# Optimization experiments

Hardware: AMD Instinct MI355X
Metric: run time of the kernel (lower is better)

Reference implementation:

```python
import jax, jax.numpy as jnp
import numpy as np

NUM_HEADS = 16
EPS = 1e-12  # matches torch F.normalize eps


def _l2norm(t):
    n = jnp.sqrt(jnp.sum(t * t, axis=-1, keepdims=True))
    return t / jnp.maximum(n, EPS)


def setup_inputs() -> dict:
    key = jax.random.key(0)
    kx, kq, kk, kv = jax.random.split(key, 4)
    B, S, E = 2, 2048, 1024
    head_dim = E // NUM_HEADS
    bound = 1.0 / np.sqrt(E)  # nn.Linear default init range
    x = jax.random.normal(kx, (B, S, E), dtype=jnp.float32)
    Wq = jax.random.uniform(kq, (E, E), dtype=jnp.float32, minval=-bound, maxval=bound)
    Wk = jax.random.uniform(kk, (E, E), dtype=jnp.float32, minval=-bound, maxval=bound)
    Wv = jax.random.uniform(kv, (E, E), dtype=jnp.float32, minval=-bound, maxval=bound)
    g_scale = jnp.asarray(np.sqrt(head_dim), dtype=jnp.float32)  # 1/d_k = sqrt(head_dim)
    return {"x": x, "Wq": Wq, "Wk": Wk, "Wv": Wv, "g_scale": g_scale}


def reference(x, Wq, Wk, Wv, g_scale):
    B, S, E = x.shape
    H = NUM_HEADS
    D = E // H
    # projections (torch Linear: x @ W.T), split heads -> [B, H, S, D]
    q = (x @ Wq.T).reshape(B, S, H, D).transpose(0, 2, 1, 3)
    k = (x @ Wk.T).reshape(B, S, H, D).transpose(0, 2, 1, 3)
    v = (x @ Wv.T).reshape(B, S, H, D).transpose(0, 2, 1, 3)
    # qk_norm branch: L2-normalize q, k then learnable scale
    q = _l2norm(q)
    k = _l2norm(k)
    scores = g_scale * jnp.einsum('bhqd,bhkd->bhqk', q, k)  # [B, H, S, S]
    attn = jax.nn.softmax(scores, axis=-1)
    # dropout p=0.0 (eval) -> identity
    out = jnp.einsum('bhqk,bhkd->bhqd', attn, v)  # [B, H, S, D]
    out = out.transpose(0, 2, 1, 3).reshape(B, S, E)
    return out
```

## Files before the change

### kernel.cpp

```cpp
#include <hip/hip_runtime.h>
#include <math.h>

#define NH 16
#define HD 64
#define SEQ 2048
#define BAT 2
#define EMB 1024
#define MTOT (BAT*SEQ)
#define NTOT (3*EMB)

typedef __attribute__((ext_vector_type(8))) short bf16x8;
typedef __attribute__((ext_vector_type(4))) float f32x4;

#define MFMA16(a,b,c) __builtin_amdgcn_mfma_f32_16x16x32_bf16(a,b,c,0,0,0)

__device__ inline short f2bf(float f) {
    union { float f; unsigned u; } x; x.f = f;
    unsigned r = (x.u + 0x7FFF + ((x.u >> 16) & 1)) >> 16;
    return (short)r;
}

__device__ inline float fast_exp2(float x) {
#if __has_builtin(__builtin_amdgcn_exp2f)
    return __builtin_amdgcn_exp2f(x);
#else
    float r; asm("v_exp_f32 %0, %1" : "=v"(r) : "v"(x)); return r;
#endif
}

__device__ inline unsigned pack2bf(float a, float b) {
    union { float f; unsigned u; } x, y; x.f = a; y.f = b;
    return __builtin_amdgcn_perm(y.u + 0x8000u, x.u + 0x8000u, 0x07060302u);
}

typedef const __attribute__((address_space(1))) void* gp_t;
typedef __attribute__((address_space(3))) void* lp_t;
__device__ inline void gload16(const void* g, void* l) {
    __builtin_amdgcn_global_load_lds((gp_t)(uintptr_t)g, (lp_t)(uintptr_t)l, 16, 0, 0);
}

__global__ __launch_bounds__(256) void prep_kernel(
    const float* __restrict__ x, const float* __restrict__ wq,
    const float* __restrict__ wk, const float* __restrict__ wv,
    short* __restrict__ xb, short* __restrict__ wb)
{
    const size_t NX = (size_t)MTOT * EMB;
    const size_t NW = (size_t)EMB * EMB;
    const size_t i4 = ((size_t)blockIdx.x * 256 + threadIdx.x) * 4;
    float4 v; short* dst;
    if (i4 < NX) { v = *(const float4*)(x + i4); dst = xb + i4; }
    else {
        size_t j = i4 - NX;
        const float* s = (j < NW) ? wq : (j < 2 * NW) ? wk : wv;
        v = *(const float4*)(s + (j & (NW - 1)));
        dst = wb + j;
    }
    short4 o; o.x = f2bf(v.x); o.y = f2bf(v.y); o.z = f2bf(v.z); o.w = f2bf(v.w);
    *(short4*)dst = o;
}

__global__ __launch_bounds__(256) void qkv_gemm_fast(
    const short* __restrict__ xb, const short* __restrict__ wb,
    short* __restrict__ qws, short* __restrict__ kws, short* __restrict__ vperm,
    const float* __restrict__ gptr)
{
    __shared__ short As[128 * 64];
    __shared__ short Bs[128 * 64];
    const int m0 = blockIdx.x * 128, n0 = blockIdx.y * 128;
    const int t = threadIdx.x, wave = t >> 6, lane = t & 63;
    const int quad = lane >> 4, l16 = lane & 15;
    const int wm = (wave & 1) * 64, wn = (wave >> 1) * 64;

    const int srow = wave * 32 + (lane >> 3);
    const int scol = ((lane & 7) ^ (srow & 7)) * 8;
    const short* ga = xb + (size_t)(m0 + srow) * EMB + scol;
    const short* gb = wb + (size_t)(n0 + srow) * EMB + scol;
    short* lA = As + (size_t)wave * 2048;
    short* lB = Bs + (size_t)wave * 2048;

    const short* Aa[2]; const short* Ba[2];
#pragma unroll
    for (int ks = 0; ks < 2; ++ks) {
        const int pc = (ks * 32 + quad * 8) ^ ((l16 & 7) * 8);
        Aa[ks] = As + (wm + l16) * 64 + pc;
        Ba[ks] = Bs + (wn + l16) * 64 + pc;
    }

    f32x4 acc[4][4] = {};

    for (int k0 = 0; k0 < EMB; k0 += 64) {
#pragma unroll
        for (int j = 0; j < 4; ++j) {
            gload16(ga + k0 + (size_t)j * 8 * EMB, lA + j * 512);
            gload16(gb + k0 + (size_t)j * 8 * EMB, lB + j * 512);
        }
        __syncthreads();
#pragma unroll
        for (int ks = 0; ks < 2; ++ks) {
            bf16x8 af[4], bfr[4];
#pragma unroll
            for (int i = 0; i < 4; ++i) af[i]  = *(const bf16x8*)(Aa[ks] + i * 1024);
#pragma unroll
            for (int i = 0; i < 4; ++i) bfr[i] = *(const bf16x8*)(Ba[ks] + i * 1024);
#pragma unroll
            for (int mf = 0; mf < 4; ++mf)
#pragma unroll
                for (int nf = 0; nf < 4; ++nf)
                    acc[mf][nf] = MFMA16(af[mf], bfr[nf], acc[mf][nf]);
        }
        __syncthreads();
    }

    const int mat = n0 >> 10;
    if (mat < 2) {
        const float scale = (mat == 0) ? gptr[0] * 1.4426950408889634f : 1.0f;
        float inv[4][4];
#pragma unroll
        for (int mf = 0; mf < 4; ++mf)
#pragma unroll
            for (int reg = 0; reg < 4; ++reg) {
                float ss = 0.f;
#pragma unroll
                for (int nf = 0; nf < 4; ++nf) { float v = acc[mf][nf][reg]; ss += v * v; }
                ss += __shfl_xor(ss, 1, 16);
                ss += __shfl_xor(ss, 2, 16);
                ss += __shfl_xor(ss, 4, 16);
                ss += __shfl_xor(ss, 8, 16);
                inv[mf][reg] = scale / fmaxf(sqrtf(ss), 1e-12f);
            }
        short* outp = (mat == 0) ? qws : kws;
#pragma unroll
        for (int mf = 0; mf < 4; ++mf)
#pragma unroll
            for (int nf = 0; nf < 4; ++nf) {
                const int cw = (n0 & 1023) + wn + nf * 16 + l16;
                const int h = cw >> 6, d = cw & 63;
#pragma unroll
                for (int reg = 0; reg < 4; ++reg) {
                    const int s = m0 + wm + mf * 16 + quad * 4 + reg;
                    const int b = s >> 11, sl = s & (SEQ - 1);
                    outp[(((size_t)(b * NH + h) * SEQ + sl) * HD) + d] =
                        f2bf(acc[mf][nf][reg] * inv[mf][reg]);
                }
            }
    } else {
#pragma unroll
        for (int mf = 0; mf < 4; ++mf)
#pragma unroll
            for (int nf = 0; nf < 4; ++nf) {
                const int cw = (n0 & 1023) + wn + nf * 16 + l16;
                const int h = cw >> 6, d = cw & 63;
                const int s = m0 + wm + mf * 16 + quad * 4;
                const int b = s >> 11, sl = s & (SEQ - 1);
                const int pos = (sl & ~31) + ((sl & 12) >> 2) * 8 + ((sl >> 4) & 1) * 4;
                short4 o;
                o.x = f2bf(acc[mf][nf][0]); o.y = f2bf(acc[mf][nf][1]);
                o.z = f2bf(acc[mf][nf][2]); o.w = f2bf(acc[mf][nf][3]);
                *(short4*)&vperm[(((size_t)(b * NH + h) * HD + d) * SEQ) + pos] = o;
            }
    }
}

__global__ __launch_bounds__(256, 3) void attn_kernel(
    const short* __restrict__ qws, const short* __restrict__ kws,
    const short* __restrict__ vperm, float* __restrict__ out)
{
    __shared__ short Kt[2][2][2048];
    __shared__ short Vt[2][2][2048];
    __shared__ float lbuf[64];

    const int id = blockIdx.x;
    const int bh = id & 31, qt = id >> 5;
    const int b = bh >> 4, h = bh & (NH - 1);
    const size_t base = (size_t)bh * SEQ * HD;
    const int t = threadIdx.x, wave = t >> 6, lane = t & 63;
    const int quad = lane >> 4, l16 = lane & 15;
    const int qh = wave >> 1, kh = wave & 1;

    bf16x8 bq[2][2];
#pragma unroll
    for (int qsub = 0; qsub < 2; ++qsub) {
        const short* qp = qws + base +
            (size_t)(qt * 64 + qh * 32 + qsub * 16 + l16) * HD + quad * 8;
        bq[qsub][0] = *(const bf16x8*)(qp);
        bq[qsub][1] = *(const bf16x8*)(qp + 32);
    }
    bf16x8 ones;
#pragma unroll
    for (int i = 0; i < 8; ++i) ones[i] = (short)0x3F80;

    int koff[2][2];
#pragma unroll
    for (int msub = 0; msub < 2; ++msub)
#pragma unroll
        for (int ks = 0; ks < 2; ++ks)
            koff[msub][ks] = (msub * 16 + l16) * 64 + (((ks * 4 + quad) ^ (l16 & 7)) * 8);
    int voff[4];
#pragma unroll
    for (int nt = 0; nt < 4; ++nt) {
        const int d = nt * 16 + l16;
        voff[nt] = d * 32 + ((quad ^ ((d >> 1) & 3)) * 8);
    }

    f32x4 o_acc[2][4] = {};
    f32x4 l_acc[2] = {};

    auto stage = [&](int tt, int p) {
        if (qh == 0) {
#pragma unroll
            for (int j = 0; j < 4; ++j) {
                const int kl = j * 8 + (lane >> 3);
                const int row = tt * 64 + kh * 32 + kl;
                gload16(kws + base + (size_t)row * HD + (((lane & 7) ^ (kl & 7)) * 8),
                        &Kt[p][kh][j * 512 + lane * 8]);
            }
        } else {
#pragma unroll
            for (int j = 0; j < 4; ++j) {
                const int d = j * 16 + (lane >> 2);
                const int ug = (lane & 3) ^ ((d >> 1) & 3);
                gload16(vperm + base + (size_t)d * SEQ + tt * 64 + kh * 32 + ug * 8,
                        &Vt[p][kh][j * 512 + lane * 8]);
            }
        }
    };

    stage(0, 0);
    __syncthreads();

    for (int tt = 0; tt < SEQ / 64; ++tt) {
        const int p = tt & 1;
        if (tt + 1 < SEQ / 64) stage(tt + 1, p ^ 1);
        const short* Kp = &Kt[p][kh][0];
        const short* Vp = &Vt[p][kh][0];

        f32x4 st[2][2];
#pragma unroll
        for (int msub = 0; msub < 2; ++msub) {
            bf16x8 a0 = *(const bf16x8*)(Kp + koff[msub][0]);
            bf16x8 a1 = *(const bf16x8*)(Kp + koff[msub][1]);
#pragma unroll
            for (int qsub = 0; qsub < 2; ++qsub) {
                f32x4 z = {};
                z = MFMA16(a0, bq[qsub][0], z);
                st[msub][qsub] = MFMA16(a1, bq[qsub][1], z);
            }
        }
        bf16x8 vf[4];
#pragma unroll
        for (int nt = 0; nt < 4; ++nt)
            vf[nt] = *(const bf16x8*)(Vp + voff[nt]);
#pragma unroll
        for (int qsub = 0; qsub < 2; ++qsub) {
            bf16x8 pa;
            unsigned* pu = (unsigned*)&pa;
            pu[0] = pack2bf(fast_exp2(st[0][qsub][0]), fast_exp2(st[0][qsub][1]));
            pu[1] = pack2bf(fast_exp2(st[0][qsub][2]), fast_exp2(st[0][qsub][3]));
            pu[2] = pack2bf(fast_exp2(st[1][qsub][0]), fast_exp2(st[1][qsub][1]));
            pu[3] = pack2bf(fast_exp2(st[1][qsub][2]), fast_exp2(st[1][qsub][3]));
            l_acc[qsub] = MFMA16(pa, ones, l_acc[qsub]);
#pragma unroll
            for (int nt = 0; nt < 4; ++nt)
                o_acc[qsub][nt] = MFMA16(pa, vf[nt], o_acc[qsub][nt]);
        }
        __syncthreads();
    }

    float* red = (float*)&Kt[0][0][0];
    if (kh == 1) {
#pragma unroll
        for (int qsub = 0; qsub < 2; ++qsub) {
#pragma unroll
            for (int nt = 0; nt < 4; ++nt)
#pragma unroll
                for (int r = 0; r < 4; ++r)
                    red[qh * 2048 + (qsub * 16 + quad * 4 + r) * 64 + nt * 16 + l16] =
                        o_acc[qsub][nt][r];
            if (l16 == 0)
#pragma unroll
                for (int r = 0; r < 4; ++r)
                    lbuf[qh * 32 + qsub * 16 + quad * 4 + r] = l_acc[qsub][r];
        }
    }
    __syncthreads();
    if (kh == 0) {
#pragma unroll
        for (int qsub = 0; qsub < 2; ++qsub) {
            float linv[4];
#pragma unroll
            for (int r = 0; r < 4; ++r)
                linv[r] = 1.0f / (l_acc[qsub][r] + lbuf[qh * 32 + qsub * 16 + quad * 4 + r]);
            const int s = qt * 64 + qh * 32 + qsub * 16 + quad * 4;
            float* ob = out + ((size_t)b * SEQ + s) * EMB + h * HD + l16;
#pragma unroll
            for (int nt = 0; nt < 4; ++nt)
#pragma unroll
                for (int r = 0; r < 4; ++r) {
                    const float o = o_acc[qsub][nt][r] +
                        red[qh * 2048 + (qsub * 16 + quad * 4 + r) * 64 + nt * 16 + l16];
                    ob[(size_t)r * EMB + nt * 16] = o * linv[r];
                }
        }
    }
}

extern "C" void kernel_launch(void* const* d_in, const int* in_sizes, int n_in,
                              void* d_out, int out_size, void* d_ws, size_t ws_size,
                              hipStream_t stream) {
    (void)in_sizes; (void)n_in; (void)out_size; (void)ws_size;
    const float* x  = (const float*)d_in[0];
    const float* Wq = (const float*)d_in[1];
    const float* Wk = (const float*)d_in[2];
    const float* Wv = (const float*)d_in[3];
    const float* g  = (const float*)d_in[4];
    float* out = (float*)d_out;

    const size_t per = (size_t)BAT * NH * SEQ * HD;
    short* qws   = (short*)d_ws;
    short* kws   = qws + per;
    short* vperm = kws + per;

    short* xb = (short*)out;
    short* wb = xb + (size_t)MTOT * EMB;

    prep_kernel<<<7168, 256, 0, stream>>>(x, Wq, Wk, Wv, xb, wb);
    qkv_gemm_fast<<<dim3(MTOT / 128, NTOT / 128), 256, 0, stream>>>(
        xb, wb, qws, kws, vperm, g);
    attn_kernel<<<(SEQ / 64) * BAT * NH, 256, 0, stream>>>(qws, kws, vperm, out);
}
```

Baseline: 164.2 us.

## Stage QKV epilogue through LDS, remap attention blocks, truncate P packing

The QKV GEMM epilogue now writes the results into a swizzled shared-memory tile and then emits coalesced 16-byte row stores for Q/K and for the permuted V layout. Before, each thread issued scattered 2-byte or 8-byte global writes. The attention kernel's launch bounds go from 3 to 4 waves per SIMD and the block-to-head mapping is remapped for locality. The probability packing switches from rounded to truncated bf16 conversion to save two adds per pair, at some accuracy cost. The extra occupancy target may force register spills.

```diff
diff --git a/kernel.cpp b/kernel.cpp
--- a/kernel.cpp
+++ b/kernel.cpp
@@ -28,9 +28,9 @@
 #endif
 }
 
-__device__ inline unsigned pack2bf(float a, float b) {
+__device__ inline unsigned pack2bf_t(float a, float b) {
     union { float f; unsigned u; } x, y; x.f = a; y.f = b;
-    return __builtin_amdgcn_perm(y.u + 0x8000u, x.u + 0x8000u, 0x07060302u);
+    return __builtin_amdgcn_perm(y.u, x.u, 0x07060302u);
 }
 
 typedef const __attribute__((address_space(1))) void* gp_t;
@@ -64,8 +64,9 @@
     short* __restrict__ qws, short* __restrict__ kws, short* __restrict__ vperm,
     const float* __restrict__ gptr)
 {
-    __shared__ short As[128 * 64];
-    __shared__ short Bs[128 * 64];
+    __shared__ short smem[2 * 128 * 64];
+    short* As = smem;
+    short* Bs = smem + 128 * 64;
     const int m0 = blockIdx.x * 128, n0 = blockIdx.y * 128;
     const int t = threadIdx.x, wave = t >> 6, lane = t & 63;
     const int quad = lane >> 4, l16 = lane & 15;
@@ -111,7 +112,9 @@
         __syncthreads();
     }
 
+    short* T = smem;
     const int mat = n0 >> 10;
+
     if (mat < 2) {
         const float scale = (mat == 0) ? gptr[0] * 1.4426950408889634f : 1.0f;
         float inv[4][4];
@@ -128,40 +131,63 @@
                 ss += __shfl_xor(ss, 8, 16);
                 inv[mf][reg] = scale / fmaxf(sqrtf(ss), 1e-12f);
             }
-        short* outp = (mat == 0) ? qws : kws;
 #pragma unroll
         for (int mf = 0; mf < 4; ++mf)
 #pragma unroll
             for (int nf = 0; nf < 4; ++nf) {
-                const int cw = (n0 & 1023) + wn + nf * 16 + l16;
-                const int h = cw >> 6, d = cw & 63;
+                const int c = wn + nf * 16 + l16;
 #pragma unroll
                 for (int reg = 0; reg < 4; ++reg) {
-                    const int s = m0 + wm + mf * 16 + quad * 4 + reg;
-                    const int b = s >> 11, sl = s & (SEQ - 1);
-                    outp[(((size_t)(b * NH + h) * SEQ + sl) * HD) + d] =
+                    const int s = wm + mf * 16 + quad * 4 + reg;
+                    T[s * 128 + (((c >> 3) ^ (s & 15)) << 3) + (c & 7)] =
                         f2bf(acc[mf][nf][reg] * inv[mf][reg]);
                 }
             }
+        __syncthreads();
+        short* outp = (mat == 0) ? qws : kws;
+        const int r = t >> 1, half = t & 1;
+        const int sg = m0 + r, bb = sg >> 11, sl = sg & (SEQ - 1);
+        const int h = ((n0 & 1023) >> 6) + half;
+        short* orow = outp + ((size_t)(bb * NH + h) * SEQ + sl) * HD;
+#pragma unroll
+        for (int j = 0; j < 8; ++j) {
+            int4 v = *(const int4*)&T[r * 128 + ((((half * 8 + j)) ^ (r & 15)) << 3)];
+            *(int4*)&orow[j * 8] = v;
+        }
     } else {
 #pragma unroll
         for (int mf = 0; mf < 4; ++mf)
 #pragma unroll
             for (int nf = 0; nf < 4; ++nf) {
-                const int cw = (n0 & 1023) + wn + nf * 16 + l16;
-                const int h = cw >> 6, d = cw & 63;
-                const int s = m0 + wm + mf * 16 + quad * 4;
-                const int b = s >> 11, sl = s & (SEQ - 1);
-                const int pos = (sl & ~31) + ((sl & 12) >> 2) * 8 + ((sl >> 4) & 1) * 4;
-                short4 o;
-                o.x = f2bf(acc[mf][nf][0]); o.y = f2bf(acc[mf][nf][1]);
-                o.z = f2bf(acc[mf][nf][2]); o.w = f2bf(acc[mf][nf][3]);
-                *(short4*)&vperm[(((size_t)(b * NH + h) * HD + d) * SEQ) + pos] = o;
-            }
-    }
-}
-
-__global__ __launch_bounds__(256, 3) void attn_kernel(
+                const int c = wn + nf * 16 + l16;
+#pragma unroll
+                for (int reg = 0; reg < 4; ++reg) {
+                    const int s = wm + mf * 16 + quad * 4 + reg;
+                    const int sp = (s & ~31) + ((s & 12) >> 2) * 8 + ((s >> 4) & 1) * 4 + (s & 3);
+                    T[sp * 128 + (((c >> 3) ^ (sp & 15)) << 3) + (c & 7)] =
+                        f2bf(acc[mf][nf][reg]);
+                }
+            }
+        __syncthreads();
+        const int c = t >> 1, half = t & 1;
+        const int h = ((n0 & 1023) >> 6) + (c >> 6), d = c & 63;
+        const int bb = m0 >> 11, p0 = (m0 & (SEQ - 1)) + half * 64;
+        short* vrow = vperm + ((size_t)(bb * NH + h) * HD + d) * SEQ + p0;
+        const int cg = c >> 3, ce = c & 7;
+#pragma unroll
+        for (int j = 0; j < 8; ++j) {
+            union { int4 v; short s[8]; } tmp;
+#pragma unroll
+            for (int e = 0; e < 8; ++e) {
+                const int s = half * 64 + j * 8 + e;
+                tmp.s[e] = T[s * 128 + ((cg ^ (s & 15)) << 3) + ce];
+            }
+            *(int4*)&vrow[j * 8] = tmp.v;
+        }
+    }
+}
+
+__global__ __launch_bounds__(256, 4) void attn_kernel(
     const short* __restrict__ qws, const short* __restrict__ kws,
     const short* __restrict__ vperm, float* __restrict__ out)
 {
@@ -170,7 +196,8 @@
     __shared__ float lbuf[64];
 
     const int id = blockIdx.x;
-    const int bh = id & 31, qt = id >> 5;
+    const int bh = (id & 7) * 4 + ((id >> 3) & 3);
+    const int qt = id >> 5;
     const int b = bh >> 4, h = bh & (NH - 1);
     const size_t base = (size_t)bh * SEQ * HD;
     const int t = threadIdx.x, wave = t >> 6, lane = t & 63;
@@ -254,10 +281,10 @@
         for (int qsub = 0; qsub < 2; ++qsub) {
             bf16x8 pa;
             unsigned* pu = (unsigned*)&pa;
-            pu[0] = pack2bf(fast_exp2(st[0][qsub][0]), fast_exp2(st[0][qsub][1]));
-            pu[1] = pack2bf(fast_exp2(st[0][qsub][2]), fast_exp2(st[0][qsub][3]));
-            pu[2] = pack2bf(fast_exp2(st[1][qsub][0]), fast_exp2(st[1][qsub][1]));
-            pu[3] = pack2bf(fast_exp2(st[1][qsub][2]), fast_exp2(st[1][qsub][3]));
+            pu[0] = pack2bf_t(fast_exp2(st[0][qsub][0]), fast_exp2(st[0][qsub][1]));
+            pu[1] = pack2bf_t(fast_exp2(st[0][qsub][2]), fast_exp2(st[0][qsub][3]));
+            pu[2] = pack2bf_t(fast_exp2(st[1][qsub][0]), fast_exp2(st[1][qsub][1]));
+            pu[3] = pack2bf_t(fast_exp2(st[1][qsub][2]), fast_exp2(st[1][qsub][3]));
             l_acc[qsub] = MFMA16(pa, ones, l_acc[qsub]);
 #pragma unroll
             for (int nt = 0; nt < 4; ++nt)
```

Result: no change. 165.9 us (+1.0%).
